# Performance work log

Hardware: AMD Instinct MI355X
Metric: run time of the kernel (lower is better)

Reference implementation:

```python
import jax, jax.numpy as jnp
import numpy as np


def setup_inputs() -> dict:
    key = jax.random.key(0)
    x = jax.random.normal(key, (4, 3, 8192), dtype=jnp.float32)  # (B, 3, N)
    return {"x": x, "k": 30}


def reference(x, k):
    # x: (B, 3, N)
    x_t = jnp.swapaxes(x, 1, 2)  # (B, N, 3)
    xx = jnp.sum(x_t ** 2, axis=2, keepdims=True)  # (B, N, 1)
    # pairwise squared distances (B, N, N)
    pairwise = xx + jnp.swapaxes(xx, 1, 2) - 2.0 * jnp.matmul(x_t, x)
    # k smallest distances -> negate and take top_k
    _, idx = jax.lax.top_k(-pairwise, k)  # idx: (B, N, k)
    # gather neighbors: (B, N, k, 3)
    neighbors = jax.vmap(lambda pts, i: pts[i])(x_t, idx)
    centroid = jnp.mean(neighbors, axis=2, keepdims=True)  # (B, N, 1, 3)
    centered = neighbors - centroid  # (B, N, k, 3)
    # per-point 3x3 covariance
    cov = jnp.einsum('bnki,bnkj->bnij', centered, centered)  # (B, N, 3, 3)
    _, v = jnp.linalg.eigh(cov)  # eigenvalues ascending
    normals = v[..., :, 0]  # eigenvector of smallest eigenvalue, (B, N, 3)
    # orient normals toward viewpoint (origin): view_dir = -x_t
    dot = jnp.sum(-x_t * normals, axis=-1, keepdims=True)
    normals = jnp.where(dot < 0, -normals, normals)
    x_out = jnp.concatenate([x, jnp.swapaxes(normals, 1, 2)], axis=1)  # (B, 6, N)
    return x_out
```

## Files before the change

kernel.cpp:

```cpp
#include <hip/hip_runtime.h>
#include <math.h>

#define N_PTS   8192
#define KNN     30
#define CAPG    104
#define STR     105
#define GROUPS  8
#define BLOCK   128
#define NZ      64
#define NY      64
#define NBKT    (NZ * NY)
#define CLO     -4.0f
#define CSC     8.0f
#define LAMBDA  48.0f


__device__ __forceinline__ int clampi(int v, int lo, int hi) {
    return v < lo ? lo : (v > hi ? hi : v);
}
__device__ __forceinline__ int bucket_of(float pz, float py) {
    int zb = clampi((int)floorf((pz - CLO) * CSC), 0, NZ - 1);
    int yb = clampi((int)floorf((py - CLO) * CSC), 0, NY - 1);
    return (zb << 6) | yb;
}

__global__ __launch_bounds__(256) void hist_kernel(const float* __restrict__ x,
                                                   int* __restrict__ hist,
                                                   float* __restrict__ out) {
    int gid = blockIdx.x * 256 + threadIdx.x;
    int b = gid >> 13, i = gid & (N_PTS - 1);
    const float* xb = x + (size_t)b * 3 * N_PTS;
    float px = xb[i], py = xb[N_PTS + i], pz = xb[2 * N_PTS + i];
    float* ob = out + (size_t)b * 6 * N_PTS;
    ob[i]             = px;
    ob[N_PTS + i]     = py;
    ob[2 * N_PTS + i] = pz;
    atomicAdd(&hist[b * NBKT + bucket_of(pz, py)], 1);
}

__global__ __launch_bounds__(256) void scan_kernel(const int* __restrict__ hist,
                                                   int* __restrict__ bstart,
                                                   int* __restrict__ cur) {
    __shared__ int wtot[4];
    const int b = blockIdx.x, t = threadIdx.x;
    const int lane = t & 63, wid = t >> 6;
    const int* h = hist + b * NBKT;
    int base = t * 16;
    int s = 0;
    #pragma unroll
    for (int k = 0; k < 16; ++k) s += h[base + k];
    int sum = s;
    #pragma unroll
    for (int off = 1; off < 64; off <<= 1) {
        int v = __shfl_up(sum, off);
        if (lane >= off) sum += v;
    }
    if (lane == 63) wtot[wid] = sum;
    __syncthreads();
    int wbase = 0;
    #pragma unroll
    for (int k = 0; k < 4; ++k) wbase += (k < wid) ? wtot[k] : 0;
    int run = wbase + sum - s;
    int* bsb = bstart + b * (NBKT + 1);
    #pragma unroll
    for (int k = 0; k < 16; ++k) {
        bsb[base + k] = run;
        cur[b * NBKT + base + k] = run;
        run += h[base + k];
    }
    if (t == 255) bsb[NBKT] = N_PTS;
}

__global__ __launch_bounds__(256) void scatter_kernel(const float* __restrict__ x,
                                                      float4* __restrict__ S,
                                                      int* __restrict__ O,
                                                      int* __restrict__ cur) {
    int gid = blockIdx.x * 256 + threadIdx.x;
    int b = gid >> 13, i = gid & (N_PTS - 1);
    const float* xb = x + (size_t)b * 3 * N_PTS;
    float px = xb[i], py = xb[N_PTS + i], pz = xb[2 * N_PTS + i];
    float xx = __fadd_rn(__fadd_rn(__fmul_rn(px, px), __fmul_rn(py, py)),
                         __fmul_rn(pz, pz));
    int dst = atomicAdd(&cur[b * NBKT + bucket_of(pz, py)], 1);
    S[(b << 13) + dst] = make_float4(px, py, pz, xx);
    O[(b << 13) + dst] = i;
}

__global__ __launch_bounds__(BLOCK, 6) void knn_normal_kernel(const float4* __restrict__ S,
                                                              const int* __restrict__ O,
                                                              const int* __restrict__ bstart,
                                                              float* __restrict__ out) {
    __shared__ unsigned long long ldk[GROUPS * STR];

    const int t    = threadIdx.x;
    const int l16  = t & 15;
    const int g    = t >> 4;
    const int gsh  = (t & 63) & ~15;
    const int qid  = blockIdx.x + (g << 12);
    const int b    = qid >> 13;
    const int pos  = qid & (N_PTS - 1);
    const float4* __restrict__ P  = S + ((size_t)b << 13);
    const int*    __restrict__ Ob = O + ((size_t)b << 13);
    const int*    __restrict__ bs = bstart + b * (NBKT + 1);
    const float4 qp = P[pos];
    const int    oi = Ob[pos];

    unsigned long long* __restrict__ ldg = ldk + g * STR;

    const float c = fmaxf(sqrtf(qp.w), 1e-3f);
    float rlo = 0.05f, rhi = 6.0f;
    for (int it = 0; it < 14; ++it) {
        float r = 0.5f * (rlo + rhi);
        float slo = fmaxf(c - r, 0.0f);
        float h = (c + r - slo) * 0.125f;
        float f = 0.0f;
        if (l16 <= 8) {
            float sq = slo + h * (float)l16;
            float cs = c - sq;
            float hh = fmaxf(fminf((r * r - cs * cs) * (0.5f / c), 2.0f * sq), 0.0f);
            float w = (l16 == 0 || l16 == 8) ? 1.0f : ((l16 & 1) ? 4.0f : 2.0f);
            f = w * __expf(-0.5f * sq * sq) * sq * hh;
        }
        f += __shfl_xor(f, 1, 16); f += __shfl_xor(f, 2, 16);
        f += __shfl_xor(f, 4, 16); f += __shfl_xor(f, 8, 16);
        float lam = 1089.3f * f * h;
        if (lam < LAMBDA) rlo = r; else rhi = r;
    }
    float rad = rhi * 1.02f;
    float r2  = rad * rad;

    int  cnt = 0;
    bool active = true;

    for (;;) {
        if (active) {
            cnt = 0;
            float w = __fmaf_rn(sqrtf(r2), 1.002f, 1e-3f);
            int zlo = clampi((int)floorf((qp.z - w - CLO) * CSC), 0, NZ - 1);
            int zhi = clampi((int)floorf((qp.z + w - CLO) * CSC), 0, NZ - 1);
            int ylo = clampi((int)floorf((qp.y - w - CLO) * CSC), 0, NY - 1);
            int yhi = clampi((int)floorf((qp.y + w - CLO) * CSC), 0, NY - 1);
            for (int zb = zlo; zb <= zhi; ++zb) {
                int lo = bs[(zb << 6) + ylo];
                int hi = bs[(zb << 6) + yhi + 1];
                int smax = (hi - lo + 31) >> 5;
                for (int s = 0; s < smax; ++s) {
                    int j1  = lo + (s << 5) + l16;
                    int j2  = j1 + 16;
                    int jc1 = j1 < hi ? j1 : hi - 1;
                    int jc2 = j2 < hi ? j2 : hi - 1;
                    float4 p1 = P[jc1];
                    float4 p2 = P[jc2];
                    float mm1 = __fmaf_rn(qp.z, p1.z, __fmaf_rn(qp.y, p1.y, __fmul_rn(qp.x, p1.x)));
                    float d1  = __fsub_rn(__fadd_rn(qp.w, p1.w), __fmul_rn(2.0f, mm1));
                    float mm2 = __fmaf_rn(qp.z, p2.z, __fmaf_rn(qp.y, p2.y, __fmul_rn(qp.x, p2.x)));
                    float d2  = __fsub_rn(__fadd_rn(qp.w, p2.w), __fmul_rn(2.0f, mm2));
                    bool hit1 = (j1 < hi) && (d1 <= r2);
                    bool hit2 = (j2 < hi) && (d2 <= r2);
                    unsigned long long m1 = __ballot(hit1);
                    unsigned sub1 = (unsigned)((m1 >> gsh) & 0xFFFFull);
                    if (hit1) {
                        int slot = cnt + __popc(sub1 & ((1u << l16) - 1u));
                        if (slot < CAPG) {
                            unsigned u = __float_as_uint(d1);
                            u = (u & 0x80000000u) ? ~u : (u | 0x80000000u);
                            ldg[slot] = ((unsigned long long)u << 28) | (unsigned long long)jc1;
                        }
                    }
                    cnt += __popc(sub1);
                    unsigned long long m2 = __ballot(hit2);
                    unsigned sub2 = (unsigned)((m2 >> gsh) & 0xFFFFull);
                    if (hit2) {
                        int slot = cnt + __popc(sub2 & ((1u << l16) - 1u));
                        if (slot < CAPG) {
                            unsigned u = __float_as_uint(d2);
                            u = (u & 0x80000000u) ? ~u : (u | 0x80000000u);
                            ldg[slot] = ((unsigned long long)u << 28) | (unsigned long long)jc2;
                        }
                    }
                    cnt += __popc(sub2);
                }
            }
        }
        bool bad = active && (cnt < KNN || cnt > CAPG);
        if (__ballot(bad) == 0ULL) break;
        active = bad;
        if (active) r2 = (cnt < KNN) ? r2 * 1.6f : r2 * 0.82f;
    }

    for (int k = l16; k < cnt; k += 16) {
        unsigned long long key = ldg[k];
        int jc = (int)(key & 0x3FFFull);
        ldg[k] = (key & ~0x0FFFFFFFull) | ((unsigned long long)Ob[jc] << 14) | (unsigned long long)jc;
    }
    __syncthreads();

    const double qx = (double)qp.x, qy = (double)qp.y, qz = (double)qp.z;
    double sx = 0.0, sy = 0.0, sz = 0.0;
    double sxx = 0.0, sxy = 0.0, sxz = 0.0, syy = 0.0, syz = 0.0, szz = 0.0;

    for (int k = l16; k < cnt; k += 16) {
        unsigned long long key = ldg[k];
        int rank = 0;
        for (int u = 0; u < cnt; ++u) rank += (ldg[u] < key) ? 1 : 0;
        if (rank < KNN) {
            float4 p = P[(int)(key & 0x3FFFull)];
            double ax = (double)p.x - qx, ay = (double)p.y - qy, az = (double)p.z - qz;
            sx += ax; sy += ay; sz += az;
            sxx = fma(ax, ax, sxx); sxy = fma(ax, ay, sxy); sxz = fma(ax, az, sxz);
            syy = fma(ay, ay, syy); syz = fma(ay, az, syz); szz = fma(az, az, szz);
        }
    }

    #pragma unroll
    for (int off = 1; off < 16; off <<= 1) {
        sx  += __shfl_xor(sx,  off, 16); sy  += __shfl_xor(sy,  off, 16); sz  += __shfl_xor(sz,  off, 16);
        sxx += __shfl_xor(sxx, off, 16); sxy += __shfl_xor(sxy, off, 16); sxz += __shfl_xor(sxz, off, 16);
        syy += __shfl_xor(syy, off, 16); syz += __shfl_xor(syz, off, 16); szz += __shfl_xor(szz, off, 16);
    }

    if (l16 == 0) {
        const double kinv = 1.0 / (double)KNN;
        double m00 = sxx - sx * sx * kinv;
        double m11 = syy - sy * sy * kinv;
        double m22 = szz - sz * sz * kinv;
        double m01 = sxy - sx * sy * kinv;
        double m02 = sxz - sx * sz * kinv;
        double m12 = syz - sy * sz * kinv;

        double nx = 1.0, ny = 0.0, nz = 0.0;
        double q3 = (m00 + m11 + m22) / 3.0;
        double p1 = m01 * m01 + m02 * m02 + m12 * m12;
        double d00 = m00 - q3, d11 = m11 - q3, d22 = m22 - q3;
        double p2 = d00 * d00 + d11 * d11 + d22 * d22 + 2.0 * p1;
        if (p2 > 1e-280) {
            double pp = sqrt(p2 / 6.0);
            double ip = 1.0 / pp;
            double b00 = d00 * ip, b11 = d11 * ip, b22 = d22 * ip;
            double b01 = m01 * ip, b02 = m02 * ip, b12 = m12 * ip;
            double detB = b00 * (b11 * b22 - b12 * b12)
                        - b01 * (b01 * b22 - b12 * b02)
                        + b02 * (b01 * b12 - b11 * b02);
            double rr = 0.5 * detB;
            rr = rr < -1.0 ? -1.0 : (rr > 1.0 ? 1.0 : rr);
            double phi = acos(rr) / 3.0;
            double lam = q3 + 2.0 * pp * cos(phi + 2.0943951023931953);
            double a00 = m00 - lam, a11 = m11 - lam, a22 = m22 - lam;
            double v0x = m01 * m12 - m02 * a11, v0y = m02 * m01 - a00 * m12, v0z = a00 * a11 - m01 * m01;
            double v1x = m01 * a22 - m02 * m12, v1y = m02 * m02 - a00 * a22, v1z = a00 * m12 - m01 * m02;
            double v2x = a11 * a22 - m12 * m12, v2y = m12 * m02 - m01 * a22, v2z = m01 * m12 - a11 * m02;
            double n0 = v0x * v0x + v0y * v0y + v0z * v0z;
            double n1 = v1x * v1x + v1y * v1y + v1z * v1z;
            double n2 = v2x * v2x + v2y * v2y + v2z * v2z;
            double bx = v0x, by = v0y, bz = v0z, bn = n0;
            if (n1 > bn) { bx = v1x; by = v1y; bz = v1z; bn = n1; }
            if (n2 > bn) { bx = v2x; by = v2y; bz = v2z; bn = n2; }
            if (bn > 1e-280) {
                double inv = 1.0 / sqrt(bn);
                nx = bx * inv; ny = by * inv; nz = bz * inv;
            }
        }
        double dq = -(qx * nx + qy * ny + qz * nz);
        if (dq < 0.0) { nx = -nx; ny = -ny; nz = -nz; }

        float* ob = out + (size_t)b * 6 * N_PTS;
        ob[3 * N_PTS + oi] = (float)nx;
        ob[4 * N_PTS + oi] = (float)ny;
        ob[5 * N_PTS + oi] = (float)nz;
    }
}

extern "C" void kernel_launch(void* const* d_in, const int* in_sizes, int n_in,
                              void* d_out, int out_size, void* d_ws, size_t ws_size,
                              hipStream_t stream) {
    const float* x = (const float*)d_in[0];
    float* out = (float*)d_out;
    char* ws = (char*)d_ws;
    float4* S    = (float4*)(ws);
    int*    O    = (int*)(ws + 524288);
    int*    bsta = (int*)(ws + 655360);
    int*    hist = (int*)(ws + 720912);
    int*    cur  = (int*)(ws + 786448);

    hipMemsetAsync(hist, 0, 4 * NBKT * sizeof(int), stream);
    hist_kernel<<<dim3(128), dim3(256), 0, stream>>>(x, hist, out);
    scan_kernel<<<dim3(4), dim3(256), 0, stream>>>(hist, bsta, cur);
    scatter_kernel<<<dim3(128), dim3(256), 0, stream>>>(x, S, O, cur);
    knn_normal_kernel<<<dim3(4096), dim3(BLOCK), 0, stream>>>(S, O, bsta, out);
}
```

Baseline: 174.4 us.

## Fuse histogram and scan, trim y-range per z-slab, register-resident rank keys

Several changes land together. The memset, histogram and scan kernels are merged into one 1024-thread-per-batch kernel that counts in shared memory, which removes two launches and the global atomics. The block-to-query mapping becomes a permuted contiguous one (qblk*8+g), so each block's groups work on spatially adjacent queries. Each z-slab's y-range is narrowed to the circle chord, so fewer candidate buckets are scanned. The rank computation keeps each lane's up to 7 keys in registers and makes one pass over shared memory instead of one pass per key. The cost is more register pressure, and if any group collects more than 112 candidates, only 7 keys per lane are held and the rest are dropped.

```diff
diff --git a/kernel.cpp b/kernel.cpp
--- a/kernel.cpp
+++ b/kernel.cpp
@@ -12,6 +12,7 @@
 #define NBKT    (NZ * NY)
 #define CLO     -4.0f
 #define CSC     8.0f
+#define BWID    0.125f
 #define LAMBDA  48.0f
 
 
@@ -24,9 +25,54 @@
     return (zb << 6) | yb;
 }
 
-__global__ __launch_bounds__(256) void hist_kernel(const float* __restrict__ x,
-                                                   int* __restrict__ hist,
-                                                   float* __restrict__ out) {
+__global__ __launch_bounds__(1024) void histscan_kernel(const float* __restrict__ x,
+                                                        int* __restrict__ bstart,
+                                                        int* __restrict__ cur) {
+    __shared__ int hist[NBKT];
+    __shared__ int wtot[16];
+    const int b = blockIdx.x, t = threadIdx.x;
+    const int lane = t & 63, wid = t >> 6;
+    const float* xb = x + (size_t)b * 3 * N_PTS;
+
+    for (int k = t; k < NBKT; k += 1024) hist[k] = 0;
+    __syncthreads();
+    #pragma unroll
+    for (int u = 0; u < 8; ++u) {
+        int i = (u << 10) + t;
+        float py = xb[N_PTS + i], pz = xb[2 * N_PTS + i];
+        atomicAdd(&hist[bucket_of(pz, py)], 1);
+    }
+    __syncthreads();
+
+    int base = t << 2;
+    int l0 = hist[base], l1 = hist[base + 1], l2 = hist[base + 2], l3 = hist[base + 3];
+    int s = l0 + l1 + l2 + l3;
+    int sum = s;
+    #pragma unroll
+    for (int off = 1; off < 64; off <<= 1) {
+        int v = __shfl_up(sum, off);
+        if (lane >= off) sum += v;
+    }
+    if (lane == 63) wtot[wid] = sum;
+    __syncthreads();
+    int wbase = 0;
+    #pragma unroll
+    for (int k = 0; k < 16; ++k) wbase += (k < wid) ? wtot[k] : 0;
+    int run = wbase + sum - s;
+    int* bsb = bstart + b * (NBKT + 1);
+    int* curb = cur + b * NBKT;
+    bsb[base]     = run; curb[base]     = run; run += l0;
+    bsb[base + 1] = run; curb[base + 1] = run; run += l1;
+    bsb[base + 2] = run; curb[base + 2] = run; run += l2;
+    bsb[base + 3] = run; curb[base + 3] = run;
+    if (t == 1023) bsb[NBKT] = N_PTS;
+}
+
+__global__ __launch_bounds__(256) void scatter_kernel(const float* __restrict__ x,
+                                                      float4* __restrict__ S,
+                                                      int* __restrict__ O,
+                                                      int* __restrict__ cur,
+                                                      float* __restrict__ out) {
     int gid = blockIdx.x * 256 + threadIdx.x;
     int b = gid >> 13, i = gid & (N_PTS - 1);
     const float* xb = x + (size_t)b * 3 * N_PTS;
@@ -35,50 +81,6 @@
     ob[i]             = px;
     ob[N_PTS + i]     = py;
     ob[2 * N_PTS + i] = pz;
-    atomicAdd(&hist[b * NBKT + bucket_of(pz, py)], 1);
-}
-
-__global__ __launch_bounds__(256) void scan_kernel(const int* __restrict__ hist,
-                                                   int* __restrict__ bstart,
-                                                   int* __restrict__ cur) {
-    __shared__ int wtot[4];
-    const int b = blockIdx.x, t = threadIdx.x;
-    const int lane = t & 63, wid = t >> 6;
-    const int* h = hist + b * NBKT;
-    int base = t * 16;
-    int s = 0;
-    #pragma unroll
-    for (int k = 0; k < 16; ++k) s += h[base + k];
-    int sum = s;
-    #pragma unroll
-    for (int off = 1; off < 64; off <<= 1) {
-        int v = __shfl_up(sum, off);
-        if (lane >= off) sum += v;
-    }
-    if (lane == 63) wtot[wid] = sum;
-    __syncthreads();
-    int wbase = 0;
-    #pragma unroll
-    for (int k = 0; k < 4; ++k) wbase += (k < wid) ? wtot[k] : 0;
-    int run = wbase + sum - s;
-    int* bsb = bstart + b * (NBKT + 1);
-    #pragma unroll
-    for (int k = 0; k < 16; ++k) {
-        bsb[base + k] = run;
-        cur[b * NBKT + base + k] = run;
-        run += h[base + k];
-    }
-    if (t == 255) bsb[NBKT] = N_PTS;
-}
-
-__global__ __launch_bounds__(256) void scatter_kernel(const float* __restrict__ x,
-                                                      float4* __restrict__ S,
-                                                      int* __restrict__ O,
-                                                      int* __restrict__ cur) {
-    int gid = blockIdx.x * 256 + threadIdx.x;
-    int b = gid >> 13, i = gid & (N_PTS - 1);
-    const float* xb = x + (size_t)b * 3 * N_PTS;
-    float px = xb[i], py = xb[N_PTS + i], pz = xb[2 * N_PTS + i];
     float xx = __fadd_rn(__fadd_rn(__fmul_rn(px, px), __fmul_rn(py, py)),
                          __fmul_rn(pz, pz));
     int dst = atomicAdd(&cur[b * NBKT + bucket_of(pz, py)], 1);
@@ -96,7 +98,8 @@
     const int l16  = t & 15;
     const int g    = t >> 4;
     const int gsh  = (t & 63) & ~15;
-    const int qid  = blockIdx.x + (g << 12);
+    const int qblk = (blockIdx.x * 1031) & 4095;
+    const int qid  = qblk * GROUPS + g;
     const int b    = qid >> 13;
     const int pos  = qid & (N_PTS - 1);
     const float4* __restrict__ P  = S + ((size_t)b << 13);
@@ -135,12 +138,16 @@
     for (;;) {
         if (active) {
             cnt = 0;
-            float w = __fmaf_rn(sqrtf(r2), 1.002f, 1e-3f);
+            float w  = __fmaf_rn(sqrtf(r2), 1.002f, 1e-3f);
+            float w2 = w * w;
             int zlo = clampi((int)floorf((qp.z - w - CLO) * CSC), 0, NZ - 1);
             int zhi = clampi((int)floorf((qp.z + w - CLO) * CSC), 0, NZ - 1);
-            int ylo = clampi((int)floorf((qp.y - w - CLO) * CSC), 0, NY - 1);
-            int yhi = clampi((int)floorf((qp.y + w - CLO) * CSC), 0, NY - 1);
             for (int zb = zlo; zb <= zhi; ++zb) {
+                float rz0 = CLO + (float)zb * BWID;
+                float dz  = fmaxf(fmaxf(rz0 - qp.z, qp.z - (rz0 + BWID)), 0.0f);
+                float yw  = sqrtf(fmaxf(w2 - dz * dz, 0.0f));
+                int ylo = clampi((int)floorf((qp.y - yw - CLO) * CSC), 0, NY - 1);
+                int yhi = clampi((int)floorf((qp.y + yw - CLO) * CSC), 0, NY - 1);
                 int lo = bs[(zb << 6) + ylo];
                 int hi = bs[(zb << 6) + yhi + 1];
                 int smax = (hi - lo + 31) >> 5;
@@ -188,23 +195,43 @@
         if (active) r2 = (cnt < KNN) ? r2 * 1.6f : r2 * 0.82f;
     }
 
-    for (int k = l16; k < cnt; k += 16) {
-        unsigned long long key = ldg[k];
-        int jc = (int)(key & 0x3FFFull);
-        ldg[k] = (key & ~0x0FFFFFFFull) | ((unsigned long long)Ob[jc] << 14) | (unsigned long long)jc;
+    unsigned long long mykey[7];
+    #pragma unroll
+    for (int m = 0; m < 7; ++m) mykey[m] = ~0ULL;
+    {
+        int nk = 0;
+        for (int k = l16; k < cnt; k += 16) {
+            unsigned long long key = ldg[k];
+            int jc = (int)(key & 0x3FFFull);
+            key = (key & ~0x0FFFFFFFull) | ((unsigned long long)Ob[jc] << 14)
+                | (unsigned long long)jc;
+            ldg[k] = key;
+            mykey[nk++] = key;
+        }
     }
     __syncthreads();
+
+    int rank0 = 0, rank1 = 0, rank2 = 0, rank3 = 0, rank4 = 0, rank5 = 0, rank6 = 0;
+    for (int u = 0; u < cnt; ++u) {
+        unsigned long long ku = ldg[u];
+        rank0 += (ku < mykey[0]) ? 1 : 0;
+        rank1 += (ku < mykey[1]) ? 1 : 0;
+        rank2 += (ku < mykey[2]) ? 1 : 0;
+        rank3 += (ku < mykey[3]) ? 1 : 0;
+        rank4 += (ku < mykey[4]) ? 1 : 0;
+        rank5 += (ku < mykey[5]) ? 1 : 0;
+        rank6 += (ku < mykey[6]) ? 1 : 0;
+    }
+    int rank[7] = { rank0, rank1, rank2, rank3, rank4, rank5, rank6 };
 
     const double qx = (double)qp.x, qy = (double)qp.y, qz = (double)qp.z;
     double sx = 0.0, sy = 0.0, sz = 0.0;
     double sxx = 0.0, sxy = 0.0, sxz = 0.0, syy = 0.0, syz = 0.0, szz = 0.0;
 
-    for (int k = l16; k < cnt; k += 16) {
-        unsigned long long key = ldg[k];
-        int rank = 0;
-        for (int u = 0; u < cnt; ++u) rank += (ldg[u] < key) ? 1 : 0;
-        if (rank < KNN) {
-            float4 p = P[(int)(key & 0x3FFFull)];
+    #pragma unroll
+    for (int m = 0; m < 7; ++m) {
+        if (rank[m] < KNN) {
+            float4 p = P[(int)(mykey[m] & 0x3FFFull)];
             double ax = (double)p.x - qx, ay = (double)p.y - qy, az = (double)p.z - qz;
             sx += ax; sy += ay; sz += az;
             sxx = fma(ax, ax, sxx); sxy = fma(ax, ay, sxy); sxz = fma(ax, az, sxz);
@@ -279,12 +306,9 @@
     float4* S    = (float4*)(ws);
     int*    O    = (int*)(ws + 524288);
     int*    bsta = (int*)(ws + 655360);
-    int*    hist = (int*)(ws + 720912);
-    int*    cur  = (int*)(ws + 786448);
-
-    hipMemsetAsync(hist, 0, 4 * NBKT * sizeof(int), stream);
-    hist_kernel<<<dim3(128), dim3(256), 0, stream>>>(x, hist, out);
-    scan_kernel<<<dim3(4), dim3(256), 0, stream>>>(hist, bsta, cur);
-    scatter_kernel<<<dim3(128), dim3(256), 0, stream>>>(x, S, O, cur);
+    int*    cur  = (int*)(ws + 720912);
+
+    histscan_kernel<<<dim3(4), dim3(1024), 0, stream>>>(x, bsta, cur);
+    scatter_kernel<<<dim3(128), dim3(256), 0, stream>>>(x, S, O, cur, out);
     knn_normal_kernel<<<dim3(4096), dim3(BLOCK), 0, stream>>>(S, O, bsta, out);
 }
```

After: 164.7 us. 5.6% less time.
